# Kernel tuning notes

Hardware: AMD Instinct MI355X
Metric: run time of the kernel (lower is better)

Reference implementation:

```python
import jax, jax.numpy as jnp
import numpy as np

TEMP_RANGE = 6   # temps 1..5
LAMBDA_1 = 1.0
LAMBDA_2 = 1.0
ALPHA = 0.7
CHUNK = 1000     # rows per block of the virtual N x N scd outer product


def setup_inputs() -> dict:
    key = jax.random.key(0)
    k1, k2, k3 = jax.random.split(key, 3)
    B, C = 64, 100
    return {
        "logits_student": jax.random.normal(k1, (B, C), dtype=jnp.float32),
        "logits_teacher": jax.random.normal(k2, (B, C), dtype=jnp.float32),
        "target": jax.random.randint(k3, (B,), 0, C),
    }


def _cube(logits):
    # stack softened softmaxes for temps 1..TEMP_RANGE-1 -> [B, C, K]
    temps = jnp.arange(1, TEMP_RANGE, dtype=logits.dtype)
    return jax.nn.softmax(logits[:, :, None] / temps[None, None, :], axis=1)


def _l1_outer_diff_sum(t, s):
    # sum_{a,b} | t_a t_b - s_a s_b |  without materializing the N x N tensor;
    # stream row-blocks of the virtual outer product via lax.scan.
    n_chunks = t.shape[0] // CHUNK
    t_blocks = t.reshape(n_chunks, CHUNK)
    s_blocks = s.reshape(n_chunks, CHUNK)

    def body(acc, xs):
        tc, sc = xs  # [CHUNK]
        blk = jnp.abs(tc[:, None] * t[None, :] - sc[:, None] * s[None, :])
        return acc + jnp.sum(blk), None

    total, _ = jax.lax.scan(body, jnp.zeros((), t.dtype), (t_blocks, s_blocks))
    return total


def _forward(logits_student, logits_teacher, target):
    # ---- KD loss (temp loop; CE term is temp-independent, matches original) ----
    log_p_s = jax.nn.log_softmax(logits_student, axis=1)
    ce = -jnp.mean(jnp.take_along_axis(log_p_s, target[:, None], axis=1))
    kd = jnp.zeros((), logits_student.dtype)
    for temp in range(1, TEMP_RANGE):
        log_q = jax.nn.log_softmax(logits_student / temp, axis=1)
        p = jax.nn.softmax(logits_teacher / temp, axis=1)
        # torch F.kl_div default reduction='mean' divides by numel (B*C)
        kl = jnp.mean(p * (jnp.log(p) - log_q))
        kd = kd + kl * (ALPHA * temp * temp) + ce * (1.0 - ALPHA)

    # ---- cubes [B, C, K] ----
    sc = _cube(logits_student)
    tc = _cube(logits_teacher)
    t = tc.reshape(-1)  # [N], N = B*C*K
    s = sc.reshape(-1)

    # ---- L2 over virtual scd = t (x) t - s (x) s : closed form ----
    tt = jnp.sum(t * t)
    ss = jnp.sum(s * s)
    ts = jnp.sum(t * s)
    loss_l2 = 0.00025 * (tt * tt - 2.0 * ts * ts + ss * ss)

    # ---- L1 over virtual scd: streamed block reduction ----
    loss_l1 = 0.00025 * _l1_outer_diff_sum(t, s)

    # ---- sub losses: nested-loop indexing collapses to Gram matrices ----
    # loss_sub1 = sum_k || T_k T_k^T - S_k S_k^T ||_F^2   (B x B per temp)
    # loss_sub2 = sum_k || T_k^T T_k - S_k^T S_k ||_F^2   (C x C per temp)
    G = jnp.einsum('ick,jck->kij', tc, tc) - jnp.einsum('ick,jck->kij', sc, sc)
    H = jnp.einsum('bik,bjk->kij', tc, tc) - jnp.einsum('bik,bjk->kij', sc, sc)
    loss_sub = LAMBDA_1 * jnp.sum(G * G) + LAMBDA_2 * jnp.sum(H * H)

    return kd + loss_l1 + loss_l2 + loss_sub


def reference(logits_student, logits_teacher, target):
    return _forward(logits_student, logits_teacher, target)
```

## Files before the change

kernel.cpp:

```cpp
#include <hip/hip_runtime.h>
#include <math.h>

#define B 64
#define C 100
#define K 5
#define N (B*C*K)
#define M 4096

#define ALPHA 0.7f
#define L1L2_SCALE 0.00025f

#define SCAN_T 256
#define PER_T (M / SCAN_T)


__device__ __forceinline__ float waveReduceSum(float v) {
    #pragma unroll
    for (int off = 32; off > 0; off >>= 1)
        v += __shfl_xor(v, off, 64);
    return v;
}
__device__ __forceinline__ float waveReduceMax(float v) {
    #pragma unroll
    for (int off = 32; off > 0; off >>= 1)
        v = fmaxf(v, __shfl_xor(v, off, 64));
    return v;
}

__device__ __forceinline__ int binOf(float x) {
    float a = fabsf(x);
    float f = log2f(fmaf(a, 1024.0f, 1.0f)) * 76.0f;
    int j = (int)f;
    j = min(j, 2047);
    return (x < 0.0f) ? (2047 - j) : (2048 + j);
}

__global__ void softmax_kd_hist_kernel(const float* __restrict__ ls,
                                       const float* __restrict__ lt,
                                       const int* __restrict__ target,
                                       float* __restrict__ t,
                                       float* __restrict__ s,
                                       float* __restrict__ acc,
                                       float* __restrict__ binT,
                                       float* __restrict__ binS) {
    int blk = blockIdx.x;
    int k = blk / B;
    int b = blk % B;
    int tid = threadIdx.x;
    float T = (float)(k + 1);
    float invT = 1.0f / T;

    const float* lsrow = ls + b * C;
    const float* ltrow = lt + b * C;

    int c0 = tid, c1 = tid + 64;
    bool h1 = (c1 < C);

    float as0 = lsrow[c0] * invT;
    float at0 = ltrow[c0] * invT;
    float as1 = h1 ? lsrow[c1] * invT : -INFINITY;
    float at1 = h1 ? ltrow[c1] * invT : -INFINITY;

    float ms = waveReduceMax(fmaxf(as0, as1));
    float mt = waveReduceMax(fmaxf(at0, at1));

    float es0 = expf(as0 - ms);
    float es1 = h1 ? expf(as1 - ms) : 0.0f;
    float et0 = expf(at0 - mt);
    float et1 = h1 ? expf(at1 - mt) : 0.0f;

    float Zs = waveReduceSum(es0 + es1);
    float Zt = waveReduceSum(et0 + et1);
    float logZs = logf(Zs), logZt = logf(Zt);
    float invZs = 1.0f / Zs, invZt = 1.0f / Zt;

    float q0 = es0 * invZs, q1 = es1 * invZs;
    float p0 = et0 * invZt, p1 = et1 * invZt;

    float lq0 = as0 - ms - logZs;
    float lp0 = at0 - mt - logZt;
    float lq1 = as1 - ms - logZs;
    float lp1 = at1 - mt - logZt;

    int rbase = (k * B + b) * C;
    float u0 = lq0 - lp0;
    t[rbase + c0] = p0;  s[rbase + c0] = q0;
    int j0 = binOf(u0);
    atomicAdd(&binT[j0], p0);
    atomicAdd(&binS[j0], q0);
    if (h1) {
        float u1 = lq1 - lp1;
        t[rbase + c1] = p1; s[rbase + c1] = q1;
        int j1 = binOf(u1);
        atomicAdd(&binT[j1], p1);
        atomicAdd(&binS[j1], q1);
    }

    float kl_part = p0 * (lp0 - lq0) + (h1 ? p1 * (lp1 - lq1) : 0.0f);
    float klr = waveReduceSum(kl_part);
    float ttr = waveReduceSum(p0 * p0 + p1 * p1);
    float ssr = waveReduceSum(q0 * q0 + q1 * q1);
    float tsr = waveReduceSum(p0 * q0 + p1 * q1);

    float cer = 0.0f;
    if (k == 0) {
        int tg = target[b];
        float cl = (c0 == tg) ? lq0 : ((h1 && c1 == tg) ? lq1 : 0.0f);
        cer = waveReduceSum(cl);
    }

    if (tid == 0) {
        atomicAdd(&acc[0], klr * (ALPHA * T * T));
        atomicAdd(&acc[2], ttr);
        atomicAdd(&acc[3], ssr);
        atomicAdd(&acc[4], tsr);
        if (k == 0) atomicAdd(&acc[1], cer);
    }
}

__global__ void gram_kernel(const float* __restrict__ t,
                            const float* __restrict__ s,
                            float* __restrict__ acc) {
    int bx = blockIdx.x;
    int tid = threadIdx.x;
    if (bx < 160) {
        int wave = tid >> 6, lane = tid & 63;
        int k = bx / 32;
        int i = (bx % 32) * 2 + wave;
        int j = lane;
        const float* Ti = t + (k * B + i) * C;
        const float* Si = s + (k * B + i) * C;
        const float* Tj = t + (k * B + j) * C;
        const float* Sj = s + (k * B + j) * C;
        float gt = 0.0f, gs = 0.0f;
        #pragma unroll 4
        for (int c = 0; c < C; c++) {
            gt = fmaf(Ti[c], Tj[c], gt);
            gs = fmaf(Si[c], Sj[c], gs);
        }
        float g = gt - gs;
        float r = waveReduceSum(g * g);
        if (lane == 0) atomicAdd(&acc[5], r);
    } else {
        int b2 = bx - 160;
        int k = b2 / C, i = b2 % C;
        int j = tid;
        __shared__ float red[2];
        float h2 = 0.0f;
        if (j < C) {
            const float* Tk = t + k * B * C;
            const float* Sk = s + k * B * C;
            float ht = 0.0f, hs = 0.0f;
            #pragma unroll 4
            for (int b = 0; b < B; b++) {
                ht = fmaf(Tk[b * C + i], Tk[b * C + j], ht);
                hs = fmaf(Sk[b * C + i], Sk[b * C + j], hs);
            }
            float h = ht - hs;
            h2 = h * h;
        }
        float r = waveReduceSum(h2);
        int wid = j >> 6;
        if ((j & 63) == 0) red[wid] = r;
        __syncthreads();
        if (tid == 0) atomicAdd(&acc[6], red[0] + red[1]);
    }
}

__global__ void __launch_bounds__(SCAN_T)
scan_dot_finalize_kernel(const float* __restrict__ binT,
                         const float* __restrict__ binS,
                         const float* __restrict__ acc,
                         float* __restrict__ out) {
    __shared__ float cT[M], cS[M];
    __shared__ float ltt[SCAN_T], lss[SCAN_T];
    __shared__ float redT[4], redS[4];
    __shared__ float totTS[2];
    int r = threadIdx.x;
    int base = r * PER_T;

    float tl[PER_T], sl[PER_T];
    float tp = 0.f, sp = 0.f;
    #pragma unroll
    for (int e = 0; e < PER_T; e++) {
        tp += binT[base + e]; tl[e] = tp;
        sp += binS[base + e]; sl[e] = sp;
    }
    ltt[r] = tp; lss[r] = sp;
    __syncthreads();
    for (int off = 1; off < SCAN_T; off <<= 1) {
        float tv = 0.f, sv = 0.f;
        if (r >= off) { tv = ltt[r - off]; sv = lss[r - off]; }
        __syncthreads();
        ltt[r] += tv; lss[r] += sv;
        __syncthreads();
    }
    float excT = ltt[r] - tp;
    float excS = lss[r] - sp;
    #pragma unroll
    for (int e = 0; e < PER_T; e++) {
        cT[base + e] = excT + (e ? tl[e-1] : 0.f);
        cS[base + e] = excS + (e ? sl[e-1] : 0.f);
    }
    if (r == SCAN_T - 1) { totTS[0] = ltt[r]; totTS[1] = lss[r]; }
    __syncthreads();

    float dT = 0.f, dS = 0.f;
    #pragma unroll
    for (int e = 0; e < PER_T; e++) {
        int m = base + e;
        float bt = tl[e] - (e ? tl[e-1] : 0.f);
        float bs = sl[e] - (e ? sl[e-1] : 0.f);
        dT = fmaf(bt, cT[4095 - m], dT);
        dS = fmaf(bs, cS[4095 - m], dS);
    }
    float rT = waveReduceSum(dT);
    float rS = waveReduceSum(dS);
    int wid = r >> 6;
    if ((r & 63) == 0) { redT[wid] = rT; redS[wid] = rS; }
    __syncthreads();

    if (r == 0) {
        float dotT = (redT[0] + redT[1]) + (redT[2] + redT[3]);
        float dotS = (redS[0] + redS[1]) + (redS[2] + redS[3]);
        float T_tot = totTS[0], S_tot = totTS[1];
        float l1sum = 2.0f * dotT - T_tot * T_tot + S_tot * S_tot - 2.0f * dotS;

        float kl = acc[0] / (float)(B * C);
        float ce = -acc[1] / (float)B;
        float kd = kl + (float)(K) * (1.0f - ALPHA) * ce;
        float tt = acc[2], ss = acc[3], ts = acc[4];
        float l2 = L1L2_SCALE * (tt * tt - 2.0f * ts * ts + ss * ss);
        float l1 = L1L2_SCALE * l1sum;
        float sub = acc[5] + acc[6];
        out[0] = kd + l1 + l2 + sub;
    }
}

extern "C" void kernel_launch(void* const* d_in, const int* in_sizes, int n_in,
                              void* d_out, int out_size, void* d_ws, size_t ws_size,
                              hipStream_t stream) {
    const float* ls = (const float*)d_in[0];
    const float* lt = (const float*)d_in[1];
    const int* tg = (const int*)d_in[2];

    float* t = (float*)d_ws;
    float* s = t + N;
    float* acc = s + N;
    float* binT = acc + 16;
    float* binS = binT + M;

    hipMemsetAsync(acc, 0, (16 + 2 * M) * sizeof(float), stream);

    softmax_kd_hist_kernel<<<K * B, 64, 0, stream>>>(ls, lt, tg, t, s, acc, binT, binS);
    gram_kernel<<<660, 128, 0, stream>>>(t, s, acc);
    scan_dot_finalize_kernel<<<1, SCAN_T, 0, stream>>>(binT, binS, acc, (float*)d_out);
}
```

Measured before the change: 97.96 us.

## Fuse softmax, Gram, histogram scan into one kernel with last-block finalize

```diff
diff --git a/kernel.cpp b/kernel.cpp
--- a/kernel.cpp
+++ b/kernel.cpp
@@ -4,14 +4,13 @@
 #define B 64
 #define C 100
 #define K 5
-#define N (B*C*K)
 #define M 4096
+#define BLK 256
+#define G_SL 51
+#define GRID_TOT (K * G_SL + 1)
 
 #define ALPHA 0.7f
 #define L1L2_SCALE 0.00025f
-
-#define SCAN_T 256
-#define PER_T (M / SCAN_T)
 
 
 __device__ __forceinline__ float waveReduceSum(float v) {
@@ -35,205 +34,222 @@
     return (x < 0.0f) ? (2047 - j) : (2048 + j);
 }
 
-__global__ void softmax_kd_hist_kernel(const float* __restrict__ ls,
-                                       const float* __restrict__ lt,
-                                       const int* __restrict__ target,
-                                       float* __restrict__ t,
-                                       float* __restrict__ s,
-                                       float* __restrict__ acc,
-                                       float* __restrict__ binT,
-                                       float* __restrict__ binS) {
-    int blk = blockIdx.x;
-    int k = blk / B;
-    int b = blk % B;
+#define ROWPAD 101
+
+__global__ void __launch_bounds__(BLK)
+ckd_fused_kernel(const float* __restrict__ ls,
+                 const float* __restrict__ lt,
+                 const int* __restrict__ target,
+                 float* __restrict__ acc,
+                 float* __restrict__ out) {
+    __shared__ float shraw[2 * B * ROWPAD];
+    __shared__ float red2[8];
     int tid = threadIdx.x;
-    float T = (float)(k + 1);
-    float invT = 1.0f / T;
-
-    const float* lsrow = ls + b * C;
-    const float* ltrow = lt + b * C;
-
-    int c0 = tid, c1 = tid + 64;
-    bool h1 = (c1 < C);
-
-    float as0 = lsrow[c0] * invT;
-    float at0 = ltrow[c0] * invT;
-    float as1 = h1 ? lsrow[c1] * invT : -INFINITY;
-    float at1 = h1 ? ltrow[c1] * invT : -INFINITY;
-
-    float ms = waveReduceMax(fmaxf(as0, as1));
-    float mt = waveReduceMax(fmaxf(at0, at1));
-
-    float es0 = expf(as0 - ms);
-    float es1 = h1 ? expf(as1 - ms) : 0.0f;
-    float et0 = expf(at0 - mt);
-    float et1 = h1 ? expf(at1 - mt) : 0.0f;
-
-    float Zs = waveReduceSum(es0 + es1);
-    float Zt = waveReduceSum(et0 + et1);
-    float logZs = logf(Zs), logZt = logf(Zt);
-    float invZs = 1.0f / Zs, invZt = 1.0f / Zt;
-
-    float q0 = es0 * invZs, q1 = es1 * invZs;
-    float p0 = et0 * invZt, p1 = et1 * invZt;
-
-    float lq0 = as0 - ms - logZs;
-    float lp0 = at0 - mt - logZt;
-    float lq1 = as1 - ms - logZs;
-    float lp1 = at1 - mt - logZt;
-
-    int rbase = (k * B + b) * C;
-    float u0 = lq0 - lp0;
-    t[rbase + c0] = p0;  s[rbase + c0] = q0;
-    int j0 = binOf(u0);
-    atomicAdd(&binT[j0], p0);
-    atomicAdd(&binS[j0], q0);
-    if (h1) {
-        float u1 = lq1 - lp1;
-        t[rbase + c1] = p1; s[rbase + c1] = q1;
-        int j1 = binOf(u1);
-        atomicAdd(&binT[j1], p1);
-        atomicAdd(&binS[j1], q1);
+    int bx = blockIdx.x;
+    int w = tid >> 6, l = tid & 63;
+    bool h1 = (l + 64) < C;
+    int c0 = l, c1 = l + 64;
+
+    if (bx < K * G_SL) {
+        int k = bx / G_SL, slice = bx % G_SL;
+        float T = (float)(k + 1);
+        float invT = 1.0f / T;
+        float (*Tk)[ROWPAD] = (float(*)[ROWPAD])shraw;
+        float (*Sk)[ROWPAD] = (float(*)[ROWPAD])(shraw + B * ROWPAD);
+
+        float kl_a = 0.f, tt_a = 0.f, ss_a = 0.f, ts_a = 0.f, ce_a = 0.f;
+        for (int b = w; b < B; b += 4) {
+            const float* lsr = ls + b * C;
+            const float* ltr = lt + b * C;
+            float as0 = lsr[c0] * invT, at0 = ltr[c0] * invT;
+            float as1 = h1 ? lsr[c1] * invT : -INFINITY;
+            float at1 = h1 ? ltr[c1] * invT : -INFINITY;
+            float ms = waveReduceMax(fmaxf(as0, as1));
+            float mt = waveReduceMax(fmaxf(at0, at1));
+            float es0 = expf(as0 - ms), es1 = h1 ? expf(as1 - ms) : 0.f;
+            float et0 = expf(at0 - mt), et1 = h1 ? expf(at1 - mt) : 0.f;
+            float Zs = waveReduceSum(es0 + es1);
+            float Zt = waveReduceSum(et0 + et1);
+            float invZs = 1.f / Zs, invZt = 1.f / Zt;
+            float q0 = es0 * invZs, q1 = es1 * invZs;
+            float p0 = et0 * invZt, p1 = et1 * invZt;
+            Tk[b][c0] = p0; Sk[b][c0] = q0;
+            if (h1) { Tk[b][c1] = p1; Sk[b][c1] = q1; }
+            if (slice == 0) {
+                float logZs = logf(Zs), logZt = logf(Zt);
+                float lq0 = as0 - ms - logZs, lp0 = at0 - mt - logZt;
+                float lq1 = as1 - ms - logZs, lp1 = at1 - mt - logZt;
+                kl_a += p0 * (lp0 - lq0) + (h1 ? p1 * (lp1 - lq1) : 0.f);
+                tt_a += p0 * p0 + p1 * p1;
+                ss_a += q0 * q0 + q1 * q1;
+                ts_a += p0 * q0 + p1 * q1;
+                if (k == 0) {
+                    int tgt = target[b];
+                    ce_a += (c0 == tgt) ? lq0 : ((h1 && c1 == tgt) ? lq1 : 0.f);
+                }
+            }
+        }
+        if (slice == 0) {
+            float klr = waveReduceSum(kl_a);
+            float ttr = waveReduceSum(tt_a);
+            float ssr = waveReduceSum(ss_a);
+            float tsr = waveReduceSum(ts_a);
+            if (l == 0) {
+                atomicAdd(&acc[0], klr * (ALPHA * T * T));
+                atomicAdd(&acc[2], ttr);
+                atomicAdd(&acc[3], ssr);
+                atomicAdd(&acc[4], tsr);
+            }
+            if (k == 0) {
+                float cer = waveReduceSum(ce_a);
+                if (l == 0) atomicAdd(&acc[1], cer);
+            }
+        }
+        __syncthreads();
+
+        float g2 = 0.f, h2 = 0.f;
+        for (int idx = slice * BLK + tid; idx < B * B + C * C; idx += G_SL * BLK) {
+            if (idx < B * B) {
+                int i = idx >> 6, j = idx & 63;
+                float gt = 0.f, gs = 0.f;
+                #pragma unroll 4
+                for (int c = 0; c < C; c++) {
+                    gt = fmaf(Tk[i][c], Tk[j][c], gt);
+                    gs = fmaf(Sk[i][c], Sk[j][c], gs);
+                }
+                float g = gt - gs;
+                g2 += g * g;
+            } else {
+                int id2 = idx - B * B;
+                int i = id2 / C, j = id2 % C;
+                float ht = 0.f, hs = 0.f;
+                #pragma unroll 4
+                for (int b = 0; b < B; b++) {
+                    ht = fmaf(Tk[b][i], Tk[b][j], ht);
+                    hs = fmaf(Sk[b][i], Sk[b][j], hs);
+                }
+                float h = ht - hs;
+                h2 += h * h;
+            }
+        }
+        float gr = waveReduceSum(g2);
+        float hr = waveReduceSum(h2);
+        if (l == 0) { red2[w] = gr; red2[4 + w] = hr; }
+        __syncthreads();
+        if (tid == 0) {
+            atomicAdd(&acc[5], (red2[0] + red2[1]) + (red2[2] + red2[3]));
+            atomicAdd(&acc[6], (red2[4] + red2[5]) + (red2[6] + red2[7]));
+        }
+    } else {
+        float* hT  = shraw;
+        float* hS  = shraw + M;
+        float* ltt = shraw + 2 * M;
+        float* lss = shraw + 2 * M + 256;
+        float* tot = shraw + 2 * M + 512;
+        float* redD = shraw + 2 * M + 514;
+        for (int i = tid; i < 2 * M; i += BLK) shraw[i] = 0.f;
+        __syncthreads();
+
+        for (int r = w; r < K * B; r += 4) {
+            int k = r >> 6, b = r & 63;
+            float invT = 1.0f / (float)(k + 1);
+            const float* lsr = ls + b * C;
+            const float* ltr = lt + b * C;
+            float as0 = lsr[c0] * invT, at0 = ltr[c0] * invT;
+            float as1 = h1 ? lsr[c1] * invT : -INFINITY;
+            float at1 = h1 ? ltr[c1] * invT : -INFINITY;
+            float ms = waveReduceMax(fmaxf(as0, as1));
+            float mt = waveReduceMax(fmaxf(at0, at1));
+            float es0 = expf(as0 - ms), es1 = h1 ? expf(as1 - ms) : 0.f;
+            float et0 = expf(at0 - mt), et1 = h1 ? expf(at1 - mt) : 0.f;
+            float Zs = waveReduceSum(es0 + es1);
+            float Zt = waveReduceSum(et0 + et1);
+            float logZs = logf(Zs), logZt = logf(Zt);
+            float p0 = et0 / Zt, p1 = et1 / Zt;
+            float q0 = es0 / Zs, q1 = es1 / Zs;
+            float u0 = (as0 - ms - logZs) - (at0 - mt - logZt);
+            int j0 = binOf(u0);
+            atomicAdd(&hT[j0], p0);
+            atomicAdd(&hS[j0], q0);
+            if (h1) {
+                float u1 = (as1 - ms - logZs) - (at1 - mt - logZt);
+                int j1 = binOf(u1);
+                atomicAdd(&hT[j1], p1);
+                atomicAdd(&hS[j1], q1);
+            }
+        }
+        __syncthreads();
+
+        const int PER_T = M / BLK;
+        int base = tid * PER_T;
+        float tl[PER_T], sl[PER_T];
+        float tp = 0.f, sp = 0.f;
+        #pragma unroll
+        for (int e = 0; e < PER_T; e++) {
+            tp += hT[base + e]; tl[e] = tp;
+            sp += hS[base + e]; sl[e] = sp;
+        }
+        ltt[tid] = tp; lss[tid] = sp;
+        __syncthreads();
+        for (int off = 1; off < BLK; off <<= 1) {
+            float tv = 0.f, sv = 0.f;
+            if (tid >= off) { tv = ltt[tid - off]; sv = lss[tid - off]; }
+            __syncthreads();
+            ltt[tid] += tv; lss[tid] += sv;
+            __syncthreads();
+        }
+        float excT = ltt[tid] - tp;
+        float excS = lss[tid] - sp;
+        #pragma unroll
+        for (int e = 0; e < PER_T; e++) {
+            hT[base + e] = excT + (e ? tl[e - 1] : 0.f);
+            hS[base + e] = excS + (e ? sl[e - 1] : 0.f);
+        }
+        if (tid == BLK - 1) { tot[0] = ltt[tid]; tot[1] = lss[tid]; }
+        __syncthreads();
+
+        float dT = 0.f, dS = 0.f;
+        #pragma unroll
+        for (int e = 0; e < PER_T; e++) {
+            int m = base + e;
+            float bt = tl[e] - (e ? tl[e - 1] : 0.f);
+            float bs = sl[e] - (e ? sl[e - 1] : 0.f);
+            dT = fmaf(bt, hT[(M - 1) - m], dT);
+            dS = fmaf(bs, hS[(M - 1) - m], dS);
+        }
+        float rT = waveReduceSum(dT);
+        float rS = waveReduceSum(dS);
+        if (l == 0) { redD[w] = rT; redD[4 + w] = rS; }
+        __syncthreads();
+        if (tid == 0) {
+            float dotT = (redD[0] + redD[1]) + (redD[2] + redD[3]);
+            float dotS = (redD[4] + redD[5]) + (redD[6] + redD[7]);
+            float T_tot = tot[0], S_tot = tot[1];
+            float l1sum = 2.f * dotT - T_tot * T_tot + S_tot * S_tot - 2.f * dotS;
+            atomicAdd(&acc[7], l1sum);
+        }
     }
 
-    float kl_part = p0 * (lp0 - lq0) + (h1 ? p1 * (lp1 - lq1) : 0.0f);
-    float klr = waveReduceSum(kl_part);
-    float ttr = waveReduceSum(p0 * p0 + p1 * p1);
-    float ssr = waveReduceSum(q0 * q0 + q1 * q1);
-    float tsr = waveReduceSum(p0 * q0 + p1 * q1);
-
-    float cer = 0.0f;
-    if (k == 0) {
-        int tg = target[b];
-        float cl = (c0 == tg) ? lq0 : ((h1 && c1 == tg) ? lq1 : 0.0f);
-        cer = waveReduceSum(cl);
-    }
-
+    __syncthreads();
     if (tid == 0) {
-        atomicAdd(&acc[0], klr * (ALPHA * T * T));
-        atomicAdd(&acc[2], ttr);
-        atomicAdd(&acc[3], ssr);
-        atomicAdd(&acc[4], tsr);
-        if (k == 0) atomicAdd(&acc[1], cer);
-    }
-}
-
-__global__ void gram_kernel(const float* __restrict__ t,
-                            const float* __restrict__ s,
-                            float* __restrict__ acc) {
-    int bx = blockIdx.x;
-    int tid = threadIdx.x;
-    if (bx < 160) {
-        int wave = tid >> 6, lane = tid & 63;
-        int k = bx / 32;
-        int i = (bx % 32) * 2 + wave;
-        int j = lane;
-        const float* Ti = t + (k * B + i) * C;
-        const float* Si = s + (k * B + i) * C;
-        const float* Tj = t + (k * B + j) * C;
-        const float* Sj = s + (k * B + j) * C;
-        float gt = 0.0f, gs = 0.0f;
-        #pragma unroll 4
-        for (int c = 0; c < C; c++) {
-            gt = fmaf(Ti[c], Tj[c], gt);
-            gs = fmaf(Si[c], Sj[c], gs);
-        }
-        float g = gt - gs;
-        float r = waveReduceSum(g * g);
-        if (lane == 0) atomicAdd(&acc[5], r);
-    } else {
-        int b2 = bx - 160;
-        int k = b2 / C, i = b2 % C;
-        int j = tid;
-        __shared__ float red[2];
-        float h2 = 0.0f;
-        if (j < C) {
-            const float* Tk = t + k * B * C;
-            const float* Sk = s + k * B * C;
-            float ht = 0.0f, hs = 0.0f;
-            #pragma unroll 4
-            for (int b = 0; b < B; b++) {
-                ht = fmaf(Tk[b * C + i], Tk[b * C + j], ht);
-                hs = fmaf(Sk[b * C + i], Sk[b * C + j], hs);
-            }
-            float h = ht - hs;
-            h2 = h * h;
-        }
-        float r = waveReduceSum(h2);
-        int wid = j >> 6;
-        if ((j & 63) == 0) red[wid] = r;
-        __syncthreads();
-        if (tid == 0) atomicAdd(&acc[6], red[0] + red[1]);
-    }
-}
-
-__global__ void __launch_bounds__(SCAN_T)
-scan_dot_finalize_kernel(const float* __restrict__ binT,
-                         const float* __restrict__ binS,
-                         const float* __restrict__ acc,
-                         float* __restrict__ out) {
-    __shared__ float cT[M], cS[M];
-    __shared__ float ltt[SCAN_T], lss[SCAN_T];
-    __shared__ float redT[4], redS[4];
-    __shared__ float totTS[2];
-    int r = threadIdx.x;
-    int base = r * PER_T;
-
-    float tl[PER_T], sl[PER_T];
-    float tp = 0.f, sp = 0.f;
-    #pragma unroll
-    for (int e = 0; e < PER_T; e++) {
-        tp += binT[base + e]; tl[e] = tp;
-        sp += binS[base + e]; sl[e] = sp;
-    }
-    ltt[r] = tp; lss[r] = sp;
-    __syncthreads();
-    for (int off = 1; off < SCAN_T; off <<= 1) {
-        float tv = 0.f, sv = 0.f;
-        if (r >= off) { tv = ltt[r - off]; sv = lss[r - off]; }
-        __syncthreads();
-        ltt[r] += tv; lss[r] += sv;
-        __syncthreads();
-    }
-    float excT = ltt[r] - tp;
-    float excS = lss[r] - sp;
-    #pragma unroll
-    for (int e = 0; e < PER_T; e++) {
-        cT[base + e] = excT + (e ? tl[e-1] : 0.f);
-        cS[base + e] = excS + (e ? sl[e-1] : 0.f);
-    }
-    if (r == SCAN_T - 1) { totTS[0] = ltt[r]; totTS[1] = lss[r]; }
-    __syncthreads();
-
-    float dT = 0.f, dS = 0.f;
-    #pragma unroll
-    for (int e = 0; e < PER_T; e++) {
-        int m = base + e;
-        float bt = tl[e] - (e ? tl[e-1] : 0.f);
-        float bs = sl[e] - (e ? sl[e-1] : 0.f);
-        dT = fmaf(bt, cT[4095 - m], dT);
-        dS = fmaf(bs, cS[4095 - m], dS);
-    }
-    float rT = waveReduceSum(dT);
-    float rS = waveReduceSum(dS);
-    int wid = r >> 6;
-    if ((r & 63) == 0) { redT[wid] = rT; redS[wid] = rS; }
-    __syncthreads();
-
-    if (r == 0) {
-        float dotT = (redT[0] + redT[1]) + (redT[2] + redT[3]);
-        float dotS = (redS[0] + redS[1]) + (redS[2] + redS[3]);
-        float T_tot = totTS[0], S_tot = totTS[1];
-        float l1sum = 2.0f * dotT - T_tot * T_tot + S_tot * S_tot - 2.0f * dotS;
-
-        float kl = acc[0] / (float)(B * C);
-        float ce = -acc[1] / (float)B;
-        float kd = kl + (float)(K) * (1.0f - ALPHA) * ce;
-        float tt = acc[2], ss = acc[3], ts = acc[4];
-        float l2 = L1L2_SCALE * (tt * tt - 2.0f * ts * ts + ss * ss);
-        float l1 = L1L2_SCALE * l1sum;
-        float sub = acc[5] + acc[6];
-        out[0] = kd + l1 + l2 + sub;
+        __threadfence();
+        int old = atomicAdd((int*)(acc + 8), 1);
+        if (old == GRID_TOT - 1) {
+            float a0 = atomicAdd(&acc[0], 0.f);
+            float a1 = atomicAdd(&acc[1], 0.f);
+            float a2 = atomicAdd(&acc[2], 0.f);
+            float a3 = atomicAdd(&acc[3], 0.f);
+            float a4 = atomicAdd(&acc[4], 0.f);
+            float a5 = atomicAdd(&acc[5], 0.f);
+            float a6 = atomicAdd(&acc[6], 0.f);
+            float a7 = atomicAdd(&acc[7], 0.f);
+            float kl = a0 / (float)(B * C);
+            float ce = -a1 / (float)B;
+            float kd = kl + (float)(K) * (1.0f - ALPHA) * ce;
+            float l2 = L1L2_SCALE * (a2 * a2 - 2.0f * a4 * a4 + a3 * a3);
+            float l1 = L1L2_SCALE * a7;
+            out[0] = kd + l1 + l2 + (a5 + a6);
+        }
     }
 }
 
@@ -244,15 +260,8 @@
     const float* lt = (const float*)d_in[1];
     const int* tg = (const int*)d_in[2];
 
-    float* t = (float*)d_ws;
-    float* s = t + N;
-    float* acc = s + N;
-    float* binT = acc + 16;
-    float* binS = binT + M;
-
-    hipMemsetAsync(acc, 0, (16 + 2 * M) * sizeof(float), stream);
-
-    softmax_kd_hist_kernel<<<K * B, 64, 0, stream>>>(ls, lt, tg, t, s, acc, binT, binS);
-    gram_kernel<<<660, 128, 0, stream>>>(t, s, acc);
-    scan_dot_finalize_kernel<<<1, SCAN_T, 0, stream>>>(binT, binS, acc, (float*)d_out);
-}
+    float* acc = (float*)d_ws;
+
+    hipMemsetAsync(acc, 0, 16 * sizeof(float), stream);
+    ckd_fused_kernel<<<GRID_TOT, BLK, 0, stream>>>(ls, lt, tg, acc, (float*)d_out);
+}
```

After: 200.4 us. 105% more time.
